# Performance work log

Hardware: AMD Instinct MI355X
Metric: run time of the kernel (lower is better)

Reference implementation:

```python
import jax, jax.numpy as jnp
import numpy as np

HIDDEN = 4096
N_HEADS = 32
N_KV_HEADS = 8
HEAD_DIM = HIDDEN // N_HEADS          # 128
GROUP = N_HEADS // N_KV_HEADS         # 4 q-heads per kv-head
Q_SIZE = N_HEADS * HEAD_DIM           # 4096
KV_SIZE = N_KV_HEADS * HEAD_DIM       # 1024
T = 2048


def setup_inputs() -> dict:
    key = jax.random.key(0)
    k1, k2, k3 = jax.random.split(key, 3)
    positions = jnp.arange(T, dtype=jnp.int64) if jax.config.jax_enable_x64 else jnp.arange(T, dtype=jnp.int32)
    hidden_states = jax.random.normal(k1, (T, HIDDEN), dtype=jnp.float32)
    # torch.nn.Linear weights: out = x @ W.T
    w_qkv = jax.random.normal(k2, (Q_SIZE + 2 * KV_SIZE, HIDDEN), dtype=jnp.float32) * 0.02
    w_o = jax.random.normal(k3, (HIDDEN, HIDDEN), dtype=jnp.float32) * 0.02
    return {"positions": positions, "hidden_states": hidden_states, "w_qkv": w_qkv, "w_o": w_o}


def reference(positions, hidden_states, w_qkv, w_o):
    del positions  # rotary is a no-op in the fake module
    t = hidden_states.shape[0]
    scaling = HEAD_DIM ** -0.5

    qkv = hidden_states @ w_qkv.T                              # [T, q+2kv]
    q, k, v = jnp.split(qkv, [Q_SIZE, Q_SIZE + KV_SIZE], axis=-1)
    # GQA mapping: q-head h uses kv-head h // GROUP (contiguous groups)
    q = q.reshape(t, N_KV_HEADS, GROUP, HEAD_DIM)              # [T, Hkv, G, d]
    k = k.reshape(t, N_KV_HEADS, HEAD_DIM)                     # [T, Hkv, d]
    v = v.reshape(t, N_KV_HEADS, HEAD_DIM)

    # Cache starts empty -> token i attends to keys 0..i (causal prefill)
    logits = jnp.einsum('tkgd,skd->kgts', q, k) * scaling      # [Hkv, G, T, T]
    causal = jnp.tril(jnp.ones((t, t), dtype=bool))            # s <= t
    logits = jnp.where(causal, logits, jnp.finfo(logits.dtype).min)
    weights = jax.nn.softmax(logits, axis=-1)
    ctx = jnp.einsum('kgts,skd->tkgd', weights, v)             # [T, Hkv, G, d]
    ctx = ctx.reshape(t, HIDDEN)
    return ctx @ w_o.T
```

## Files before the change

kernel.cpp:

```cpp
#include <hip/hip_runtime.h>

typedef unsigned short u16;
typedef __bf16 bf16x8 __attribute__((ext_vector_type(8)));
typedef float f32x4 __attribute__((ext_vector_type(4)));

__device__ __forceinline__ u16 f2bf(float f) {
  union { float f; unsigned u; } v; v.f = f;
  unsigned r = v.u + 0x7FFFu + ((v.u >> 16) & 1u);
  return (u16)(r >> 16);
}

__device__ __forceinline__ void gload16(const void* g, void* l) {
  __builtin_amdgcn_global_load_lds(
      (const __attribute__((address_space(1))) unsigned int*)g,
      (__attribute__((address_space(3))) unsigned int*)l, 16, 0, 0);
}

__global__ __launch_bounds__(256) void cvt_bf16(const float* __restrict__ in,
                                                u16* __restrict__ out, long n) {
  long i = ((long)blockIdx.x * 256 + threadIdx.x) * 8;
  const long stride = (long)gridDim.x * 2048;
  for (; i < n; i += stride) {
    float4 a = *(const float4*)(in + i);
    float4 b = *(const float4*)(in + i + 4);
    uint4 o;
    o.x = (unsigned)f2bf(a.x) | ((unsigned)f2bf(a.y) << 16);
    o.y = (unsigned)f2bf(a.z) | ((unsigned)f2bf(a.w) << 16);
    o.z = (unsigned)f2bf(b.x) | ((unsigned)f2bf(b.y) << 16);
    o.w = (unsigned)f2bf(b.z) | ((unsigned)f2bf(b.w) << 16);
    *(uint4*)(out + i) = o;
  }
}

template <int BM, int BN, typename OUT>
__global__ __launch_bounds__(512, 2) void gemmT(const u16* __restrict__ A,
                                                const u16* __restrict__ B,
                                                OUT* __restrict__ C,
                                                int M, int N, int K) {
  constexpr int MREP = BM / 32;
  constexpr int NREP = BN / 64;
  constexpr int MPP = MREP / 4;
  constexpr int AI = BM / 64;
  constexpr int BI = BN / 64;
  __shared__ __align__(16) u16 sA[2][BM * 64];
  __shared__ __align__(16) u16 sB[2][BN * 64];

  const int tid = threadIdx.x;
  const int w = tid >> 6, ln = tid & 63;
  const int lr = ln & 15, lg = ln >> 4;
  const int wr = w >> 2, wc = w & 3;

  const int nN = N / BN;
  const int bm = (blockIdx.x / nN) * BM;
  const int bn = (blockIdx.x % nN) * BN;

  const int srow = tid >> 3;
  const int scol = (((tid & 7) * 16) ^ ((srow & 7) << 4)) >> 1;
  const u16* pA = A + (size_t)(bm + srow) * K + scol;
  const u16* pB = B + (size_t)(bn + srow) * K + scol;

  const int mask = (lr & 7) << 4;
  const int pAr = (wr * (BM / 2) + lr) * 128;
  const int pBr = (wc * (BN / 4) + lr) * 128;

  f32x4 acc[MREP][NREP] = {};
  const int nk = K >> 6;

  auto stage = [&](int buf, int t) {
    const int k0 = t << 6;
#pragma unroll
    for (int i = 0; i < AI; ++i)
      gload16(pA + (size_t)i * 64 * K + k0, (char*)sA[buf] + i * 8192 + tid * 16);
#pragma unroll
    for (int i = 0; i < BI; ++i)
      gload16(pB + (size_t)i * 64 * K + k0, (char*)sB[buf] + i * 8192 + tid * 16);
  };

  stage(0, 0);

#pragma unroll 1
  for (int t = 0; t < nk; ++t) {
    const int buf = t & 1;
    const char* lA = (const char*)sA[buf];
    const char* lB = (const char*)sB[buf];

    asm volatile("s_waitcnt vmcnt(0)" ::: "memory");
    __builtin_amdgcn_s_barrier();
    __builtin_amdgcn_sched_barrier(0);

    if (t + 1 < nk) stage(buf ^ 1, t + 1);

    bf16x8 bfr[NREP][2];
#pragma unroll
    for (int nf = 0; nf < NREP; ++nf)
#pragma unroll
      for (int s = 0; s < 2; ++s)
        bfr[nf][s] = *(const bf16x8*)(lB + pBr + nf * 2048 +
                                      ((lg * 16 + s * 64) ^ mask));

#pragma unroll
    for (int p = 0; p < 4; ++p) {
      if (p) __builtin_amdgcn_s_barrier();
      bf16x8 af[MPP][2];
#pragma unroll
      for (int m = 0; m < MPP; ++m)
#pragma unroll
        for (int s = 0; s < 2; ++s)
          af[m][s] = *(const bf16x8*)(lA + pAr + (p * MPP + m) * 2048 +
                                      ((lg * 16 + s * 64) ^ mask));
      asm volatile("s_waitcnt lgkmcnt(0)" ::: "memory");
      __builtin_amdgcn_sched_barrier(0);
      __builtin_amdgcn_s_setprio(1);
#pragma unroll
      for (int s = 0; s < 2; ++s)
#pragma unroll
        for (int m = 0; m < MPP; ++m)
#pragma unroll
          for (int nf = 0; nf < NREP; ++nf)
            acc[p * MPP + m][nf] = __builtin_amdgcn_mfma_f32_16x16x32_bf16(
                af[m][s], bfr[nf][s], acc[p * MPP + m][nf], 0, 0, 0);
      __builtin_amdgcn_s_setprio(0);
    }
  }

#pragma unroll
  for (int m = 0; m < MREP; ++m)
#pragma unroll
    for (int nf = 0; nf < NREP; ++nf)
#pragma unroll
      for (int r = 0; r < 4; ++r) {
        const int row = bm + wr * (BM / 2) + m * 16 + lg * 4 + r;
        const int col = bn + wc * (BN / 4) + nf * 16 + lr;
        const float v = acc[m][nf][r];
        if constexpr (sizeof(OUT) == 2)
          C[(size_t)row * N + col] = (OUT)f2bf(v);
        else
          C[(size_t)row * N + col] = v;
      }
}

__global__ __launch_bounds__(256) void vtrans(const u16* __restrict__ qkv,
                                              u16* __restrict__ vT) {
  __shared__ u16 tile[128][65];
  const int hk = blockIdx.y;
  const int tb = blockIdx.x * 64;
  const int tid = threadIdx.x;
#pragma unroll
  for (int p = 0; p < 4; ++p) {
    const int tr = p * 16 + (tid >> 4);
    const int d0 = (tid & 15) * 8;
    const uint4 x = *(const uint4*)(qkv + (size_t)(tb + tr) * 6144 + 5120 + hk * 128 + d0);
    const u16* xv = (const u16*)&x;
#pragma unroll
    for (int j = 0; j < 8; ++j) tile[d0 + j][tr] = xv[j];
  }
  __syncthreads();
#pragma unroll
  for (int p = 0; p < 4; ++p) {
    const int d = p * 32 + (tid >> 3);
    const int t0 = (tid & 7) * 8;
    u16 v[8];
#pragma unroll
    for (int j = 0; j < 8; ++j) v[j] = tile[d][t0 + j];
    uint4 o;
    unsigned* ov = (unsigned*)&o;
#pragma unroll
    for (int j = 0; j < 4; ++j)
      ov[j] = (unsigned)v[2 * j] | ((unsigned)v[2 * j + 1] << 16);
    *(uint4*)(vT + (size_t)hk * 128 * 2048 + (size_t)d * 2048 + tb + t0) = o;
  }
}

__global__ __launch_bounds__(256) void attn(const u16* __restrict__ qkv,
                                            const u16* __restrict__ vT,
                                            u16* __restrict__ ctx) {
  __shared__ __align__(16) u16 sK[2][64 * 128];
  __shared__ __align__(16) u16 sV[2][128 * 64];
  __shared__ __align__(16) u16 sP[4 * 16 * 64];
  const int tid = threadIdx.x, w = tid >> 6, ln = tid & 63;
  const int lr = ln & 15, lg = ln >> 4;
  const int h = blockIdx.y, hk = h >> 2;
  const int pi = blockIdx.x;

  const float scale = 0.08838834764831845f;
  const float LOG2E = 1.4426950408889634f;
  char* const pw = (char*)sP + w * 2048;

  auto stage = [&](int buf, int kt) {
    const int kvbase = kt * 64;
#pragma unroll
    for (int i = 0; i < 4; ++i) {
      const int off = i * 4096 + tid * 16;
      {
        const int row = off >> 8, cbp = off & 255;
        const int cb = cbp ^ ((row & 7) << 4);
        gload16(qkv + (size_t)(kvbase + row) * 6144 + 4096 + hk * 128 + (cb >> 1),
                (char*)sK + buf * 16384 + off);
      }
      {
        const int row = off >> 7, cbp = off & 127;
        const int cb = cbp ^ ((row & 7) << 4);
        gload16(vT + (size_t)hk * 262144 + (size_t)row * 2048 + kvbase + (cb >> 1),
                (char*)sV + buf * 16384 + off);
      }
    }
  };

#pragma unroll 1
  for (int ph = 0; ph < 2; ++ph) {
    const int qt = ph ? (31 - pi) : pi;
    const int qbase = qt * 64;
    const int nkt = qt + 1;

    bf16x8 qf[4];
    {
      const u16* qrow = qkv + (size_t)(qbase + w * 16 + lr) * 6144 + h * 128 + lg * 8;
#pragma unroll
      for (int kk = 0; kk < 4; ++kk) qf[kk] = *(const bf16x8*)(qrow + kk * 32);
    }

    f32x4 acc_o[8] = {};
    float m_r[4] = {-INFINITY, -INFINITY, -INFINITY, -INFINITY};
    float l_r[4] = {0.f, 0.f, 0.f, 0.f};

    stage(0, 0);

#pragma unroll 1
    for (int kt = 0; kt < nkt; ++kt) {
      const int buf = kt & 1;
      const int kvbase = kt * 64;
      __syncthreads();
      if (kt + 1 < nkt) stage(buf ^ 1, kt + 1);

      char* const kbase = (char*)sK + buf * 16384;
      char* const vbase = (char*)sV + buf * 16384;

      f32x4 sacc[4] = {};
#pragma unroll
      for (int kk = 0; kk < 4; ++kk) {
#pragma unroll
        for (int nf = 0; nf < 4; ++nf) {
          const int row = nf * 16 + lr;
          const int byt = row * 256 + ((kk * 64 + lg * 16) ^ ((row & 7) << 4));
          const bf16x8 kf = *(const bf16x8*)(kbase + byt);
          sacc[nf] = __builtin_amdgcn_mfma_f32_16x16x32_bf16(qf[kk], kf, sacc[nf], 0, 0, 0);
        }
      }

      const bool diag = (kt == qt);
      float p[4][4];
#pragma unroll
      for (int r = 0; r < 4; ++r) {
        const int qrow = qbase + w * 16 + lg * 4 + r;
        float mx = -INFINITY;
#pragma unroll
        for (int nf = 0; nf < 4; ++nf) {
          float v = sacc[nf][r] * scale;
          if (diag && (kvbase + nf * 16 + lr > qrow)) v = -INFINITY;
          p[nf][r] = v;
          mx = fmaxf(mx, v);
        }
        mx = fmaxf(mx, __shfl_xor(mx, 1));
        mx = fmaxf(mx, __shfl_xor(mx, 2));
        mx = fmaxf(mx, __shfl_xor(mx, 4));
        mx = fmaxf(mx, __shfl_xor(mx, 8));
        const float mt = fmaxf(m_r[r], mx);
        const float alpha = exp2f((m_r[r] - mt) * LOG2E);
        m_r[r] = mt;
        float rs = 0.f;
#pragma unroll
        for (int nf = 0; nf < 4; ++nf) {
          const float e = exp2f((p[nf][r] - mt) * LOG2E);
          p[nf][r] = e;
          rs += e;
        }
        rs += __shfl_xor(rs, 1);
        rs += __shfl_xor(rs, 2);
        rs += __shfl_xor(rs, 4);
        rs += __shfl_xor(rs, 8);
        l_r[r] = l_r[r] * alpha + rs;
#pragma unroll
        for (int o = 0; o < 8; ++o) acc_o[o][r] = acc_o[o][r] * alpha;
      }

#pragma unroll
      for (int r = 0; r < 4; ++r) {
        const int row = lg * 4 + r;
#pragma unroll
        for (int nf = 0; nf < 4; ++nf) {
          const int col = nf * 16 + lr;
          const int byt = row * 128 + ((2 * col) ^ ((row & 7) << 4));
          *(u16*)(pw + byt) = f2bf(p[nf][r]);
        }
      }

#pragma unroll
      for (int kk2 = 0; kk2 < 2; ++kk2) {
        const int pbyt = lr * 128 + ((kk2 * 64 + lg * 16) ^ ((lr & 7) << 4));
        const bf16x8 pf = *(const bf16x8*)(pw + pbyt);
#pragma unroll
        for (int o = 0; o < 8; ++o) {
          const int vrow = o * 16 + lr;
          const int vbyt = vrow * 128 + ((kk2 * 64 + lg * 16) ^ ((vrow & 7) << 4));
          const bf16x8 vf = *(const bf16x8*)(vbase + vbyt);
          acc_o[o] = __builtin_amdgcn_mfma_f32_16x16x32_bf16(pf, vf, acc_o[o], 0, 0, 0);
        }
      }
    }

#pragma unroll
    for (int r = 0; r < 4; ++r) {
      const float inv = 1.f / l_r[r];
      const int t = qbase + w * 16 + lg * 4 + r;
#pragma unroll
      for (int o = 0; o < 8; ++o)
        ctx[(size_t)t * 4096 + h * 128 + o * 16 + lr] = f2bf(acc_o[o][r] * inv);
    }
    __syncthreads();
  }
}

extern "C" void kernel_launch(void* const* d_in, const int* in_sizes, int n_in,
                              void* d_out, int out_size, void* d_ws, size_t ws_size,
                              hipStream_t stream) {
  (void)in_sizes; (void)n_in; (void)out_size; (void)ws_size;
  const float* hidden = (const float*)d_in[1];
  const float* w_qkv = (const float*)d_in[2];
  const float* w_o = (const float*)d_in[3];
  float* out = (float*)d_out;
  char* ws = (char*)d_ws;

  u16* xb    = (u16*)(ws + 0);
  u16* wqkvb = (u16*)(ws + 16777216);
  u16* wob   = (u16*)(ws + 67108864);
  u16* qkvb  = (u16*)(ws + 100663296);
  u16* vTb   = (u16*)(ws + 125829120);
  u16* ctxb  = (u16*)(ws + 130023424);

  cvt_bf16<<<4096, 256, 0, stream>>>(hidden, xb, (long)2048 * 4096);
  cvt_bf16<<<8192, 256, 0, stream>>>(w_qkv, wqkvb, (long)6144 * 4096);
  cvt_bf16<<<8192, 256, 0, stream>>>(w_o, wob, (long)4096 * 4096);
  gemmT<256, 192, u16><<<256, 512, 0, stream>>>(xb, wqkvb, qkvb, 2048, 6144, 4096);
  vtrans<<<dim3(32, 8), 256, 0, stream>>>(qkvb, vTb);
  attn<<<dim3(16, 32), 256, 0, stream>>>(qkvb, vTb, ctxb);
  gemmT<128, 256, float><<<256, 512, 0, stream>>>(ctxb, wob, out, 2048, 4096, 4096);
}
```

Measured before the change: 380.3 us.

## Pre-pack weights into MFMA fragment layout and load B directly to registers

Weight conversion now writes bf16 weights in a fragment-major packed layout, so each wave can load its B operands straight from global memory into registers with coalesced 16-byte loads. This removes the B tile from shared memory. The A tile stays in LDS with double buffering, and B fragments are register double-buffered, with staged vmcnt waits to overlap loads and MFMA. The cost is higher register pressure (launch_bounds no longer requests 2 blocks per CU) and B reuse across the two wave-rows now depends on cache rather than LDS.

```diff
diff --git a/kernel.cpp b/kernel.cpp
--- a/kernel.cpp
+++ b/kernel.cpp
@@ -32,18 +32,33 @@
   }
 }
 
+__global__ __launch_bounds__(256) void pack_b(const float* __restrict__ w,
+                                              u16* __restrict__ out, int kb32) {
+  const int tid = threadIdx.x;
+  const int unit = blockIdx.x * 4 + (tid >> 6);
+  const int ln = tid & 63, lr = ln & 15, lg = ln >> 4;
+  const int n16 = unit / kb32, k32 = unit % kb32;
+  const float* src = w + (size_t)(n16 * 16 + lr) * (kb32 * 32) + k32 * 32 + lg * 8;
+  float4 a = *(const float4*)src;
+  float4 b = *(const float4*)(src + 4);
+  uint4 o;
+  o.x = (unsigned)f2bf(a.x) | ((unsigned)f2bf(a.y) << 16);
+  o.y = (unsigned)f2bf(a.z) | ((unsigned)f2bf(a.w) << 16);
+  o.z = (unsigned)f2bf(b.x) | ((unsigned)f2bf(b.y) << 16);
+  o.w = (unsigned)f2bf(b.z) | ((unsigned)f2bf(b.w) << 16);
+  *(uint4*)(out + (size_t)unit * 512 + ln * 8) = o;
+}
+
 template <int BM, int BN, typename OUT>
-__global__ __launch_bounds__(512, 2) void gemmT(const u16* __restrict__ A,
-                                                const u16* __restrict__ B,
-                                                OUT* __restrict__ C,
-                                                int M, int N, int K) {
+__global__ __launch_bounds__(512) void gemmS(const u16* __restrict__ A,
+                                             const u16* __restrict__ Bp,
+                                             OUT* __restrict__ C,
+                                             int M, int N, int K) {
   constexpr int MREP = BM / 32;
   constexpr int NREP = BN / 64;
-  constexpr int MPP = MREP / 4;
   constexpr int AI = BM / 64;
-  constexpr int BI = BN / 64;
+  constexpr int NB = NREP * 2;
   __shared__ __align__(16) u16 sA[2][BM * 64];
-  __shared__ __align__(16) u16 sB[2][BN * 64];
 
   const int tid = threadIdx.x;
   const int w = tid >> 6, ln = tid & 63;
@@ -51,76 +66,93 @@
   const int wr = w >> 2, wc = w & 3;
 
   const int nN = N / BN;
-  const int bm = (blockIdx.x / nN) * BM;
-  const int bn = (blockIdx.x % nN) * BN;
+  const int bm = ((int)blockIdx.x / nN) * BM;
+  const int bn = ((int)blockIdx.x % nN) * BN;
 
   const int srow = tid >> 3;
   const int scol = (((tid & 7) * 16) ^ ((srow & 7) << 4)) >> 1;
   const u16* pA = A + (size_t)(bm + srow) * K + scol;
-  const u16* pB = B + (size_t)(bn + srow) * K + scol;
 
   const int mask = (lr & 7) << 4;
-  const int pAr = (wr * (BM / 2) + lr) * 128;
-  const int pBr = (wc * (BN / 4) + lr) * 128;
+  const int kb32 = K >> 5;
+  const u16* pB = Bp + ((size_t)(bn / 16 + wc * NREP) * kb32) * 512 + ln * 8;
 
   f32x4 acc[MREP][NREP] = {};
   const int nk = K >> 6;
 
-  auto stage = [&](int buf, int t) {
+  auto stageA = [&](int buf, int t) {
     const int k0 = t << 6;
 #pragma unroll
     for (int i = 0; i < AI; ++i)
       gload16(pA + (size_t)i * 64 * K + k0, (char*)sA[buf] + i * 8192 + tid * 16);
-#pragma unroll
-    for (int i = 0; i < BI; ++i)
-      gload16(pB + (size_t)i * 64 * K + k0, (char*)sB[buf] + i * 8192 + tid * 16);
   };
-
-  stage(0, 0);
+  auto loadB = [&](bf16x8 (&br)[NREP][2], int t) {
+#pragma unroll
+    for (int nf = 0; nf < NREP; ++nf)
+#pragma unroll
+      for (int s = 0; s < 2; ++s)
+        br[nf][s] = *(const bf16x8*)(pB + ((size_t)nf * kb32 + 2 * t + s) * 512);
+  };
+  auto compute = [&](const char* lA, bf16x8 (&br)[NREP][2]) {
+    bf16x8 af[MREP][2];
+#pragma unroll
+    for (int m = 0; m < MREP; ++m)
+      af[m][0] = *(const bf16x8*)(lA + (wr * (BM / 2) + m * 16 + lr) * 128 +
+                                  ((lg * 16) ^ mask));
+#pragma unroll
+    for (int m = 0; m < MREP; ++m)
+      af[m][1] = *(const bf16x8*)(lA + (wr * (BM / 2) + m * 16 + lr) * 128 +
+                                  ((lg * 16 + 64) ^ mask));
+    asm volatile("s_waitcnt lgkmcnt(%0)" :: "n"(MREP) : "memory");
+    __builtin_amdgcn_sched_barrier(0);
+    __builtin_amdgcn_s_setprio(1);
+#pragma unroll
+    for (int m = 0; m < MREP; ++m)
+#pragma unroll
+      for (int nf = 0; nf < NREP; ++nf)
+        acc[m][nf] = __builtin_amdgcn_mfma_f32_16x16x32_bf16(
+            af[m][0], br[nf][0], acc[m][nf], 0, 0, 0);
+    __builtin_amdgcn_s_setprio(0);
+    asm volatile("s_waitcnt lgkmcnt(0)" ::: "memory");
+    __builtin_amdgcn_sched_barrier(0);
+    __builtin_amdgcn_s_setprio(1);
+#pragma unroll
+    for (int m = 0; m < MREP; ++m)
+#pragma unroll
+      for (int nf = 0; nf < NREP; ++nf)
+        acc[m][nf] = __builtin_amdgcn_mfma_f32_16x16x32_bf16(
+            af[m][1], br[nf][1], acc[m][nf], 0, 0, 0);
+    __builtin_amdgcn_s_setprio(0);
+  };
+
+  bf16x8 b0[NREP][2], b1[NREP][2];
+  stageA(0, 0);
+  loadB(b0, 0);
 
 #pragma unroll 1
-  for (int t = 0; t < nk; ++t) {
-    const int buf = t & 1;
-    const char* lA = (const char*)sA[buf];
-    const char* lB = (const char*)sB[buf];
-
-    asm volatile("s_waitcnt vmcnt(0)" ::: "memory");
+  for (int t = 0; t < nk; t += 2) {
+    asm volatile("s_waitcnt vmcnt(%0)" :: "n"(NB) : "memory");
+    __builtin_amdgcn_sched_barrier(0);
     __builtin_amdgcn_s_barrier();
     __builtin_amdgcn_sched_barrier(0);
-
-    if (t + 1 < nk) stage(buf ^ 1, t + 1);
-
-    bf16x8 bfr[NREP][2];
-#pragma unroll
-    for (int nf = 0; nf < NREP; ++nf)
-#pragma unroll
-      for (int s = 0; s < 2; ++s)
-        bfr[nf][s] = *(const bf16x8*)(lB + pBr + nf * 2048 +
-                                      ((lg * 16 + s * 64) ^ mask));
-
-#pragma unroll
-    for (int p = 0; p < 4; ++p) {
-      if (p) __builtin_amdgcn_s_barrier();
-      bf16x8 af[MPP][2];
-#pragma unroll
-      for (int m = 0; m < MPP; ++m)
-#pragma unroll
-        for (int s = 0; s < 2; ++s)
-          af[m][s] = *(const bf16x8*)(lA + pAr + (p * MPP + m) * 2048 +
-                                      ((lg * 16 + s * 64) ^ mask));
-      asm volatile("s_waitcnt lgkmcnt(0)" ::: "memory");
-      __builtin_amdgcn_sched_barrier(0);
-      __builtin_amdgcn_s_setprio(1);
-#pragma unroll
-      for (int s = 0; s < 2; ++s)
-#pragma unroll
-        for (int m = 0; m < MPP; ++m)
-#pragma unroll
-          for (int nf = 0; nf < NREP; ++nf)
-            acc[p * MPP + m][nf] = __builtin_amdgcn_mfma_f32_16x16x32_bf16(
-                af[m][s], bfr[nf][s], acc[p * MPP + m][nf], 0, 0, 0);
-      __builtin_amdgcn_s_setprio(0);
-    }
+    const bool m1 = (t + 1 < nk);
+    if (m1) { stageA(1, t + 1); loadB(b1, t + 1); }
+    if (m1) asm volatile("s_waitcnt vmcnt(%0)" :: "n"(AI + NB) : "memory");
+    else    asm volatile("s_waitcnt vmcnt(0)" ::: "memory");
+    __builtin_amdgcn_sched_barrier(0);
+    compute((const char*)sA[0], b0);
+
+    if (!m1) break;
+    asm volatile("s_waitcnt vmcnt(%0)" :: "n"(NB) : "memory");
+    __builtin_amdgcn_sched_barrier(0);
+    __builtin_amdgcn_s_barrier();
+    __builtin_amdgcn_sched_barrier(0);
+    const bool m2 = (t + 2 < nk);
+    if (m2) { stageA(0, t + 2); loadB(b0, t + 2); }
+    if (m2) asm volatile("s_waitcnt vmcnt(%0)" :: "n"(AI + NB) : "memory");
+    else    asm volatile("s_waitcnt vmcnt(0)" ::: "memory");
+    __builtin_amdgcn_sched_barrier(0);
+    compute((const char*)sA[1], b1);
   }
 
 #pragma unroll
@@ -331,17 +363,17 @@
   char* ws = (char*)d_ws;
 
   u16* xb    = (u16*)(ws + 0);
-  u16* wqkvb = (u16*)(ws + 16777216);
-  u16* wob   = (u16*)(ws + 67108864);
+  u16* wqkvp = (u16*)(ws + 16777216);
+  u16* wop   = (u16*)(ws + 67108864);
   u16* qkvb  = (u16*)(ws + 100663296);
   u16* vTb   = (u16*)(ws + 125829120);
   u16* ctxb  = (u16*)(ws + 130023424);
 
   cvt_bf16<<<4096, 256, 0, stream>>>(hidden, xb, (long)2048 * 4096);
-  cvt_bf16<<<8192, 256, 0, stream>>>(w_qkv, wqkvb, (long)6144 * 4096);
-  cvt_bf16<<<8192, 256, 0, stream>>>(w_o, wob, (long)4096 * 4096);
-  gemmT<256, 192, u16><<<256, 512, 0, stream>>>(xb, wqkvb, qkvb, 2048, 6144, 4096);
+  pack_b<<<12288, 256, 0, stream>>>(w_qkv, wqkvp, 128);
+  pack_b<<<8192, 256, 0, stream>>>(w_o, wop, 128);
+  gemmS<256, 192, u16><<<256, 512, 0, stream>>>(xb, wqkvp, qkvb, 2048, 6144, 4096);
   vtrans<<<dim3(32, 8), 256, 0, stream>>>(qkvb, vTb);
   attn<<<dim3(16, 32), 256, 0, stream>>>(qkvb, vTb, ctxb);
-  gemmT<128, 256, float><<<256, 512, 0, stream>>>(ctxb, wob, out, 2048, 4096, 4096);
-}
+  gemmS<128, 256, float><<<256, 512, 0, stream>>>(ctxb, wop, out, 2048, 4096, 4096);
+}
```

Result: faster. 335.0 us (-11.9%).
